# Performance work log

Hardware: AMD Instinct MI355X
Metric: run time of the kernel (lower is better)

The kernel has to match this reference:

```python
import jax, jax.numpy as jnp
import numpy as np

DIM = 1024
HEADS = 16
DIM_HEAD = 64
INNER = HEADS * DIM_HEAD
ALPHA = 128.0
SCALE = DIM_HEAD ** -0.5 / ALPHA
EPS = 1e-5
MAX_NEG = -jnp.finfo(jnp.float32).max


def layernorm(x, g):
    # torch.var(unbiased=False) layernorm with learned gain, no bias
    mean = jnp.mean(x, axis=-1, keepdims=True)
    var = jnp.mean(jnp.square(x - mean), axis=-1, keepdims=True)
    return (x - mean) * jax.lax.rsqrt(var + EPS) * g


def setup_inputs() -> dict:
    key = jax.random.key(0)
    ks = jax.random.split(key, 8)
    b, n = 8, 1024
    x = jax.random.normal(ks[0], (b, n, DIM), dtype=jnp.float32)
    mask = jax.random.bernoulli(ks[1], 0.9, (b, n))  # bool padding mask
    g_in = jnp.ones((DIM,), jnp.float32)
    Wq = jax.random.normal(ks[2], (INNER, DIM), jnp.float32) * (DIM ** -0.5)
    Wkv = jax.random.normal(ks[3], (2 * DIM_HEAD, DIM), jnp.float32) * (DIM ** -0.5)
    null_kv = jax.random.normal(ks[4], (2, DIM_HEAD), jnp.float32)
    Wo = jax.random.normal(ks[5], (DIM, INNER), jnp.float32) * (INNER ** -0.5)
    g_out = jnp.ones((DIM,), jnp.float32)
    return {"x": x, "mask": mask, "g_in": g_in, "Wq": Wq, "Wkv": Wkv,
            "null_kv": null_kv, "Wo": Wo, "g_out": g_out}


def reference(x, mask, g_in, Wq, Wkv, null_kv, Wo, g_out):
    b, n, _ = x.shape
    context = x                      # context captured BEFORE norm
    xn = layernorm(x, g_in)
    q = (xn @ Wq.T).reshape(b, n, HEADS, DIM_HEAD).transpose(0, 2, 1, 3)  # b h n d
    q = q * SCALE
    kv = context @ Wkv.T             # b n 2d (single shared KV head: MQA)
    k, v = jnp.split(kv, 2, axis=-1)
    nk = jnp.broadcast_to(null_kv[0], (b, 1, DIM_HEAD))
    nv = jnp.broadcast_to(null_kv[1], (b, 1, DIM_HEAD))
    k = jnp.concatenate([nk, k], axis=1)   # b (n+1) d
    v = jnp.concatenate([nv, v], axis=1)
    sim = jnp.einsum('bhid,bjd->bhij', q, k)  # b h n (n+1)
    # padding mask, True prepended for null token
    m = jnp.pad(mask, ((0, 0), (1, 0)), constant_values=True)
    sim = jnp.where(m[:, None, None, :], sim, MAX_NEG)
    # causal mask: triu with offset j-i+1 = 2 (null token always visible)
    i, j = n, n + 1
    causal = jnp.triu(jnp.ones((i, j), bool), j - i + 1)
    sim = jnp.where(causal, MAX_NEG, sim)
    # pb-relax: subtract detached max, rescale by alpha, softmax
    sim = sim - jax.lax.stop_gradient(jnp.max(sim, axis=-1, keepdims=True))
    attn = jax.nn.softmax(sim * ALPHA, axis=-1)
    out = jnp.einsum('bhij,bjd->bhid', attn, v)
    out = out.transpose(0, 2, 1, 3).reshape(b, n, INNER)
    out = out @ Wo.T
    return layernorm(out, g_out)
```

## Files before the change

kernel.cpp:

```cpp
#include <hip/hip_runtime.h>
#include <hip/hip_bf16.h>

#define B_     8
#define N_     1024
#define DIM_   1024
#define HEADS_ 16
#define DH_    64
#define INNER_ 1024
#define NKEY_  1025
#define NTILE_ 33
#define NW_    33
#define ROWS_  8192
#define EPS_   1e-5f
#define QK_SCALE_ 0.1803368801111f
#define TILE_ELEMS_ 4096

typedef unsigned short u16;
typedef unsigned char  u8;
typedef unsigned int   u32;
typedef __attribute__((ext_vector_type(8)))  short bf16x8;
typedef __attribute__((ext_vector_type(4)))  float f32x4;
typedef __attribute__((ext_vector_type(16))) float f32x16;

__device__ __forceinline__ float bf2f(u16 u) {
    unsigned int x = ((unsigned int)u) << 16;
    return __uint_as_float(x);
}
__device__ __forceinline__ u16 f2bf(float f) {
    unsigned int x = __float_as_uint(f);
    x += 0x7FFFu + ((x >> 16) & 1u);
    return (u16)(x >> 16);
}
__device__ __forceinline__ float max3f(float a, float b, float c) {
    return fmaxf(fmaxf(a, b), c);
}
__device__ __forceinline__ float exp2fast(float x) {
    float r;
    asm("v_exp_f32 %0, %1" : "=v"(r) : "v"(x));
    return r;
}

#define MFMA16(a, b, c) __builtin_amdgcn_mfma_f32_16x16x32_bf16((a), (b), (c), 0, 0, 0)
#define MFMA32(a, b, c) __builtin_amdgcn_mfma_f32_32x32x16_bf16((a), (b), (c), 0, 0, 0)

__device__ __forceinline__ void gload16(const void* g, void* l) {
    __builtin_amdgcn_global_load_lds(
        (const __attribute__((address_space(1))) unsigned int*)g,
        (__attribute__((address_space(3))) unsigned int*)l, 16, 0, 0);
}

__device__ __forceinline__ u32 cvtpk(float lo, float hi) {
    u32 r;
    asm("v_cvt_pk_bf16_f32 %0, %1, %2" : "=v"(r) : "v"(lo), "v"(hi));
    return r;
}
__device__ __forceinline__ void plswap(u32& a, u32& b) {
    asm volatile("v_permlane32_swap_b32 %0, %1" : "+v"(a), "+v"(b));
}

__global__ void detect_mask(const unsigned int* __restrict__ m, int* __restrict__ flag) {
    if (threadIdx.x == 0 && blockIdx.x == 0) {
        int f = 0;
        for (int i = 0; i < 64; ++i) {
            unsigned int w = m[i];
            if (w == 0x3F800000u) { f = 2; break; }
            if (w > 1u) f = 1;
        }
        *flag = f;
    }
}

__global__ void build_bits(const void* __restrict__ mraw, const int* __restrict__ flag,
                           u32* __restrict__ vbits) {
    int tid = blockIdx.x * blockDim.x + threadIdx.x;
    if (tid >= B_ * NW_) return;
    int b = tid / NW_, wq = tid - b * NW_;
    int f = *flag;
    u32 bits = 0;
    for (int i = 0; i < 32; ++i) {
        int jp = wq * 32 + i;
        bool vis;
        if (jp == 0) vis = true;
        else if (jp < NKEY_) {
            int idx = b * N_ + jp - 1;
            if (f == 0)      vis = ((const int*)mraw)[idx] != 0;
            else if (f == 1) vis = ((const u8*)mraw)[idx] != 0;
            else             vis = ((const float*)mraw)[idx] != 0.0f;
        } else vis = false;
        if (vis) bits |= (1u << i);
    }
    vbits[tid] = bits;
}

__global__ void cvt_w(const float* __restrict__ wq, const float* __restrict__ wkv,
                      const float* __restrict__ wo, u16* __restrict__ q16,
                      u16* __restrict__ kv16, u16* __restrict__ o16) {
    int i = blockIdx.x * blockDim.x + threadIdx.x;
    const int NQ = INNER_ * DIM_ / 4, NKV = 128 * DIM_ / 4, NO = DIM_ * INNER_ / 4;
    const float* src; u16* dst; int off;
    if (i < NQ)            { src = wq;  dst = q16;  off = i; }
    else if (i < NQ + NKV) { src = wkv; dst = kv16; off = i - NQ; }
    else if (i < NQ + NKV + NO) { src = wo; dst = o16; off = i - NQ - NKV; }
    else return;
    float4 v = ((const float4*)src)[off];
    ushort4 u; u.x = f2bf(v.x); u.y = f2bf(v.y); u.z = f2bf(v.z); u.w = f2bf(v.w);
    ((ushort4*)dst)[off] = u;
}

template<int MODE>
__global__ __launch_bounds__(256)
void ln_rows(const void* __restrict__ xv, const float* __restrict__ g,
             void* __restrict__ outv, u16* __restrict__ raw16) {
    int row = blockIdx.x;
    int t = threadIdx.x;
    float v0, v1, v2, v3;
    if constexpr (MODE == 0) {
        float4 v = ((const float4*)((const float*)xv + (size_t)row * DIM_))[t];
        v0 = v.x; v1 = v.y; v2 = v.z; v3 = v.w;
    } else {
        ushort4 u = ((const ushort4*)((const u16*)xv + (size_t)row * DIM_))[t];
        v0 = bf2f(u.x); v1 = bf2f(u.y); v2 = bf2f(u.z); v3 = bf2f(u.w);
    }
    float s  = v0 + v1 + v2 + v3;
    float ss = v0*v0 + v1*v1 + v2*v2 + v3*v3;
#pragma unroll
    for (int off = 32; off > 0; off >>= 1) {
        s  += __shfl_down(s,  off, 64);
        ss += __shfl_down(ss, off, 64);
    }
    __shared__ float red[10];
    int wid = t >> 6, lane = t & 63;
    if (lane == 0) { red[wid] = s; red[4 + wid] = ss; }
    __syncthreads();
    if (t == 0) {
        float S  = red[0] + red[1] + red[2] + red[3];
        float SS = red[4] + red[5] + red[6] + red[7];
        float mean = S * (1.0f / DIM_);
        float var  = SS * (1.0f / DIM_) - mean * mean;
        red[8] = mean;
        red[9] = rsqrtf(var + EPS_);
    }
    __syncthreads();
    float mean = red[8], rs = red[9];
    float4 gv = ((const float4*)g)[t];
    float o0 = (v0 - mean) * rs * gv.x;
    float o1 = (v1 - mean) * rs * gv.y;
    float o2 = (v2 - mean) * rs * gv.z;
    float o3 = (v3 - mean) * rs * gv.w;
    if constexpr (MODE == 0) {
        ushort4 u; u.x = f2bf(o0); u.y = f2bf(o1); u.z = f2bf(o2); u.w = f2bf(o3);
        ((ushort4*)((u16*)outv + (size_t)row * DIM_))[t] = u;
        ushort4 rw; rw.x = f2bf(v0); rw.y = f2bf(v1); rw.z = f2bf(v2); rw.w = f2bf(v3);
        ((ushort4*)(raw16 + (size_t)row * DIM_))[t] = rw;
    } else {
        float4 u; u.x = o0; u.y = o1; u.z = o2; u.w = o3;
        ((float4*)((float*)outv + (size_t)row * DIM_))[t] = u;
    }
}

__global__ __launch_bounds__(256)
void proj_fused(const u16* __restrict__ xn, const u16* __restrict__ xraw,
                const u16* __restrict__ wq, const u16* __restrict__ wkv,
                u16* __restrict__ qout, float* __restrict__ kvout) {
    __shared__ u16 As[128 * 32];
    __shared__ u16 Bs[128 * 32];
    const bool iskv = (blockIdx.x == 8);
    const u16* A  = iskv ? xraw : xn;
    const u16* Bt = iskv ? wkv : wq;
    const int  n0 = iskv ? 0 : blockIdx.x * 128;
    const float scale = iskv ? 1.0f : QK_SCALE_;
    const int t = threadIdx.x;
    const int w = t >> 6, l = t & 63;
    const int col = l & 15, rg = l >> 4;
    const int wm = (w >> 1) * 64, wn = (w & 1) * 64;
    const int m0 = blockIdx.y * 128;
    const int slr = l >> 2;
    const int slc = (l & 3) * 8;
    f32x4 acc[4][4];
#pragma unroll
    for (int i = 0; i < 4; ++i)
#pragma unroll
        for (int j = 0; j < 4; ++j) acc[i][j] = f32x4{0.f, 0.f, 0.f, 0.f};

    const u16* Abase = A  + (size_t)m0 * DIM_;
    const u16* Bbase = Bt + (size_t)n0 * DIM_;
    for (int k0 = 0; k0 < DIM_; k0 += 32) {
        __syncthreads();
#pragma unroll
        for (int p = 0; p < 2; ++p) {
            int rb = w * 2 + p;
            gload16(Abase + (size_t)(rb * 16 + slr) * DIM_ + k0 + slc, &As[rb * 512]);
            gload16(Bbase + (size_t)(rb * 16 + slr) * DIM_ + k0 + slc, &Bs[rb * 512]);
        }
        __syncthreads();
        bf16x8 af[4], bf4[4];
#pragma unroll
        for (int mi = 0; mi < 4; ++mi)
            af[mi] = *(const bf16x8*)&As[(wm + mi * 16 + col) * 32 + rg * 8];
#pragma unroll
        for (int ni = 0; ni < 4; ++ni)
            bf4[ni] = *(const bf16x8*)&Bs[(wn + ni * 16 + col) * 32 + rg * 8];
#pragma unroll
        for (int mi = 0; mi < 4; ++mi)
#pragma unroll
            for (int ni = 0; ni < 4; ++ni)
                acc[mi][ni] = MFMA16(af[mi], bf4[ni], acc[mi][ni]);
    }
#pragma unroll
    for (int mi = 0; mi < 4; ++mi)
#pragma unroll
        for (int ni = 0; ni < 4; ++ni)
#pragma unroll
            for (int r = 0; r < 4; ++r) {
                size_t row = (size_t)(m0 + wm + mi * 16 + rg * 4 + r);
                int c = n0 + wn + ni * 16 + col;
                float vv = acc[mi][ni][r] * scale;
                if (iskv) kvout[row * 128 + c] = vv;
                else      qout[row * INNER_ + c] = f2bf(vv);
            }
}

__global__ __launch_bounds__(256)
void gemm_o(const u16* __restrict__ A, const u16* __restrict__ Bt,
            u16* __restrict__ Cv) {
    __shared__ u16 As[128 * 32];
    __shared__ u16 Bs[128 * 32];
    const int t = threadIdx.x;
    const int w = t >> 6, l = t & 63;
    const int col = l & 15, rg = l >> 4;
    const int wm = (w >> 1) * 64, wn = (w & 1) * 64;
    const int m0 = blockIdx.y * 128, n0 = blockIdx.x * 128;
    const int slr = l >> 2;
    const int slc = (l & 3) * 8;
    f32x4 acc[4][4];
#pragma unroll
    for (int i = 0; i < 4; ++i)
#pragma unroll
        for (int j = 0; j < 4; ++j) acc[i][j] = f32x4{0.f, 0.f, 0.f, 0.f};
    const u16* Abase = A  + (size_t)m0 * INNER_;
    const u16* Bbase = Bt + (size_t)n0 * INNER_;
    for (int k0 = 0; k0 < INNER_; k0 += 32) {
        __syncthreads();
#pragma unroll
        for (int p = 0; p < 2; ++p) {
            int rb = w * 2 + p;
            gload16(Abase + (size_t)(rb * 16 + slr) * INNER_ + k0 + slc, &As[rb * 512]);
            gload16(Bbase + (size_t)(rb * 16 + slr) * INNER_ + k0 + slc, &Bs[rb * 512]);
        }
        __syncthreads();
        bf16x8 af[4], bf4[4];
#pragma unroll
        for (int mi = 0; mi < 4; ++mi)
            af[mi] = *(const bf16x8*)&As[(wm + mi * 16 + col) * 32 + rg * 8];
#pragma unroll
        for (int ni = 0; ni < 4; ++ni)
            bf4[ni] = *(const bf16x8*)&Bs[(wn + ni * 16 + col) * 32 + rg * 8];
#pragma unroll
        for (int mi = 0; mi < 4; ++mi)
#pragma unroll
            for (int ni = 0; ni < 4; ++ni)
                acc[mi][ni] = MFMA16(af[mi], bf4[ni], acc[mi][ni]);
    }
#pragma unroll
    for (int mi = 0; mi < 4; ++mi)
#pragma unroll
        for (int ni = 0; ni < 4; ++ni)
#pragma unroll
            for (int r = 0; r < 4; ++r) {
                size_t row = (size_t)(m0 + wm + mi * 16 + rg * 4 + r);
                int c = n0 + wn + ni * 16 + col;
                Cv[row * DIM_ + c] = f2bf(acc[mi][ni][r]);
            }
}

__global__ __launch_bounds__(256)
void build_kv(const float* __restrict__ kvf, const float* __restrict__ nullkv,
              u16* __restrict__ KVt) {
    const int kt = blockIdx.x, b = blockIdx.y;
    const int t = threadIdx.x;
    const int k0 = kt * 32;
    u16* base = KVt + ((size_t)b * NTILE_ + kt) * TILE_ELEMS_;
    {
        int j = t >> 3;
        int d0 = (t & 7) * 8;
        int jp = k0 + j;
        float v[8];
        if (jp == 0) {
#pragma unroll
            for (int i = 0; i < 8; ++i) v[i] = nullkv[d0 + i];
        } else if (jp <= N_) {
            const float* r = kvf + ((size_t)b * N_ + jp - 1) * 128 + d0;
            float4 a = ((const float4*)r)[0], c = ((const float4*)r)[1];
            v[0]=a.x; v[1]=a.y; v[2]=a.z; v[3]=a.w; v[4]=c.x; v[5]=c.y; v[6]=c.z; v[7]=c.w;
        } else {
#pragma unroll
            for (int i = 0; i < 8; ++i) v[i] = 0.f;
        }
        ushort4 u0, u1;
        u0.x=f2bf(v[0]); u0.y=f2bf(v[1]); u0.z=f2bf(v[2]); u0.w=f2bf(v[3]);
        u1.x=f2bf(v[4]); u1.y=f2bf(v[5]); u1.z=f2bf(v[6]); u1.w=f2bf(v[7]);
        *(ushort4*)(base + j * 64 + d0)     = u0;
        *(ushort4*)(base + j * 64 + d0 + 4) = u1;
    }
    {
        int d = t >> 2;
        int j0 = (t & 3) * 8;
        u16 o8[8];
#pragma unroll
        for (int i = 0; i < 8; ++i) {
            int jp = k0 + j0 + i;
            float val = 0.f;
            if (jp == 0) val = nullkv[64 + d];
            else if (jp <= N_) val = kvf[((size_t)b * N_ + jp - 1) * 128 + 64 + d];
            o8[i] = f2bf(val);
        }
        u16* dst = base + 2048 + d * 32 + j0;
        ushort4 u0, u1;
        u0.x=o8[0]; u0.y=o8[1]; u0.z=o8[2]; u0.w=o8[3];
        u1.x=o8[4]; u1.y=o8[5]; u1.z=o8[6]; u1.w=o8[7];
        *(ushort4*)dst = u0;
        *(ushort4*)(dst + 4) = u1;
    }
}

__device__ __forceinline__ void softmax_pv(
    f32x16& s, float& m, float& lsum, f32x16& o0, f32x16& o1,
    bool caus, int lim, const bf16x8* vf)
{
    float t0 = max3f(s[0],  s[1],  s[2]);
    float t1 = max3f(s[3],  s[4],  s[5]);
    float t2 = max3f(s[6],  s[7],  s[8]);
    float t3 = max3f(s[9],  s[10], s[11]);
    float t4 = max3f(s[12], s[13], s[14]);
    float mt = max3f(max3f(t0, t1, t2), max3f(t3, t4, s[15]), -3.0e38f);
    mt = fmaxf(mt, __shfl_xor(mt, 32, 64));
    if (!__all(mt <= m + 8.0f)) {
        float mn = fmaxf(m, mt);
        float c = exp2fast(m - mn);
        lsum *= c;
#pragma unroll
        for (int i = 0; i < 16; ++i) { o0[i] *= c; o1[i] *= c; }
        m = mn;
    }
    float p[16];
#pragma unroll
    for (int r = 0; r < 16; ++r) p[r] = exp2fast(s[r] - m);
    if (caus) {
#pragma unroll
        for (int r = 0; r < 16; ++r)
            if (((r & 3) + 8 * (r >> 2)) > lim) p[r] = 0.f;
    }
    float ls = (((p[0]+p[1])+(p[2]+p[3])) + ((p[4]+p[5])+(p[6]+p[7])))
             + (((p[8]+p[9])+(p[10]+p[11])) + ((p[12]+p[13])+(p[14]+p[15])));
    ls += __shfl_xor(ls, 32, 64);
    lsum += ls;
    u32 w0 = cvtpk(p[0],  p[1]),  w2 = cvtpk(p[4],  p[5]);  plswap(w0, w2);
    u32 w1 = cvtpk(p[2],  p[3]),  w3 = cvtpk(p[6],  p[7]);  plswap(w1, w3);
    u32 w4 = cvtpk(p[8],  p[9]),  w6 = cvtpk(p[12], p[13]); plswap(w4, w6);
    u32 w5 = cvtpk(p[10], p[11]), w7 = cvtpk(p[14], p[15]); plswap(w5, w7);
    union { u32 wd[4]; bf16x8 v; } f0, f1;
    f0.wd[0] = w0; f0.wd[1] = w1; f0.wd[2] = w2; f0.wd[3] = w3;
    f1.wd[0] = w4; f1.wd[1] = w5; f1.wd[2] = w6; f1.wd[3] = w7;
    __builtin_amdgcn_s_setprio(1);
    o0 = MFMA32(vf[0], f0.v, o0);
    o0 = MFMA32(vf[1], f1.v, o0);
    o1 = MFMA32(vf[2], f0.v, o1);
    o1 = MFMA32(vf[3], f1.v, o1);
    __builtin_amdgcn_s_setprio(0);
}

__device__ __forceinline__ void write_o(u16* __restrict__ Out, int b, int i0, int lo,
                                        int hi, int h, float lsum,
                                        const f32x16& o0, const f32x16& o1) {
    float inv = 1.0f / lsum;
    u16* ob = Out + ((size_t)(b * N_ + i0 + lo)) * INNER_ + h * DH_;
#pragma unroll
    for (int dd = 0; dd < 2; ++dd)
#pragma unroll
        for (int g = 0; g < 4; ++g) {
            int d0 = dd * 32 + 8 * g + 4 * hi;
            float e0 = (dd ? o1[4*g+0] : o0[4*g+0]) * inv;
            float e1 = (dd ? o1[4*g+1] : o0[4*g+1]) * inv;
            float e2 = (dd ? o1[4*g+2] : o0[4*g+2]) * inv;
            float e3 = (dd ? o1[4*g+3] : o0[4*g+3]) * inv;
            ushort4 u; u.x = f2bf(e0); u.y = f2bf(e1); u.z = f2bf(e2); u.w = f2bf(e3);
            *(ushort4*)(ob + d0) = u;
        }
}

__global__ __launch_bounds__(256)
void attn_un(const u16* __restrict__ Q, const u16* __restrict__ KVt,
             const u32* __restrict__ vbits, u16* __restrict__ Out) {
    const int t = threadIdx.x;
    const int w = t >> 6, l = t & 63;
    const int lo = l & 31, hi = l >> 5;
    const int fid = blockIdx.x;
    const int qt = 31 - (fid >> 5);
    const int rem = fid & 31;
    const int b = rem >> 2, hg = rem & 3;
    const int h = hg * 4 + w;
    const int i0 = qt * 32;
    const int nt = qt + 2;

    bf16x8 qf[4];
    {
        const u16* qp = Q + ((size_t)(b * N_ + i0 + lo)) * INNER_ + h * DH_ + hi * 8;
#pragma unroll
        for (int dt = 0; dt < 4; ++dt) qf[dt] = *(const bf16x8*)(qp + dt * 16);
    }
    f32x16 o0, o1;
#pragma unroll
    for (int i = 0; i < 16; ++i) { o0[i] = 0.f; o1[i] = 0.f; }
    float m = -3.0e38f, lsum = 0.f;

    const u16* tbase = KVt + (size_t)b * NTILE_ * TILE_ELEMS_;
    const u32* vbp = vbits + b * NW_;
    const int koff  = lo * 64 + hi * 8;
    const int voff0 = 2048 + lo * 32 + hi * 8;
    const int voff1 = 2048 + (lo + 32) * 32 + hi * 8;

    for (int kt = 0; kt < nt; ++kt) {
        const u16* tb = tbase + (size_t)kt * TILE_ELEMS_;
        bf16x8 kf[4], vf[4];
        kf[0] = *(const bf16x8*)(tb + koff);
        kf[1] = *(const bf16x8*)(tb + koff + 16);
        kf[2] = *(const bf16x8*)(tb + koff + 32);
        kf[3] = *(const bf16x8*)(tb + koff + 48);
        vf[0] = *(const bf16x8*)(tb + voff0);
        vf[1] = *(const bf16x8*)(tb + voff0 + 16);
        vf[2] = *(const bf16x8*)(tb + voff1);
        vf[3] = *(const bf16x8*)(tb + voff1 + 16);

        u32 vb = vbp[kt];
        union { u32 wd[4]; bf16x8 v; } bias, ones;
        bias.wd[0] = (hi == 0 && !((vb >> lo) & 1u)) ? 0xC6E0u : 0u;
        bias.wd[1] = 0; bias.wd[2] = 0; bias.wd[3] = 0;
        ones.wd[0] = (hi == 0) ? 0x3F80u : 0u;
        ones.wd[1] = 0; ones.wd[2] = 0; ones.wd[3] = 0;

        f32x16 s;
        __builtin_amdgcn_s_setprio(1);
#pragma unroll
        for (int i = 0; i < 16; ++i) s[i] = 0.f;
        s = MFMA32(kf[0], qf[0], s);
        s = MFMA32(kf[1], qf[1], s);
        s = MFMA32(kf[2], qf[2], s);
        s = MFMA32(kf[3], qf[3], s);
        s = MFMA32(bias.v, ones.v, s);
        __builtin_amdgcn_s_setprio(0);
        int lim = i0 + lo + 1 - kt * 32 - 4 * hi;
        softmax_pv(s, m, lsum, o0, o1, kt >= qt, lim, vf);
    }

    write_o(Out, b, i0, lo, hi, h, lsum, o0, o1);
}

extern "C" void kernel_launch(void* const* d_in, const int* in_sizes, int n_in,
                              void* d_out, int out_size, void* d_ws, size_t ws_size,
                              hipStream_t stream) {
    const float* x       = (const float*)d_in[0];
    const void*  maskraw = d_in[1];
    const float* g_in    = (const float*)d_in[2];
    const float* Wq      = (const float*)d_in[3];
    const float* Wkv     = (const float*)d_in[4];
    const float* nullkv  = (const float*)d_in[5];
    const float* Wo      = (const float*)d_in[6];
    const float* g_out   = (const float*)d_in[7];
    float* out = (float*)d_out;

    char* ws = (char*)d_ws;
    size_t off = 0;
    auto alloc = [&](size_t bytes) {
        void* p = ws + off;
        off += (bytes + 255) & ~(size_t)255;
        return p;
    };
    int* flag   = (int*)alloc(4);
    u32* vbits  = (u32*)alloc((size_t)B_ * NW_ * 4);
    u16* wq16   = (u16*)alloc((size_t)INNER_ * DIM_ * 2);
    u16* wkv16  = (u16*)alloc((size_t)128 * DIM_ * 2);
    u16* wo16   = (u16*)alloc((size_t)DIM_ * INNER_ * 2);
    u16* bufA   = (u16*)alloc((size_t)ROWS_ * DIM_ * 2);
    u16* xb     = (u16*)alloc((size_t)ROWS_ * DIM_ * 2);
    u16* bufC   = (u16*)alloc((size_t)ROWS_ * INNER_ * 2);
    float* kvf  = (float*)alloc((size_t)ROWS_ * 128 * 4);
    u16* KVt    = (u16*)alloc((size_t)B_ * NTILE_ * TILE_ELEMS_ * 2);

    detect_mask<<<1, 64, 0, stream>>>((const unsigned int*)maskraw, flag);
    build_bits<<<2, 256, 0, stream>>>(maskraw, flag, vbits);

    cvt_w<<<2176, 256, 0, stream>>>(Wq, Wkv, Wo, wq16, wkv16, wo16);

    ln_rows<0><<<ROWS_, 256, 0, stream>>>(x, g_in, bufA, xb);

    proj_fused<<<dim3(9, ROWS_ / 128), 256, 0, stream>>>(
        bufA, xb, wq16, wkv16, bufC, kvf);

    build_kv<<<dim3(NTILE_, B_), 256, 0, stream>>>(kvf, nullkv, KVt);

    attn_un<<<1024, 256, 0, stream>>>(bufC, KVt, vbits, bufA);

    gemm_o<<<dim3(DIM_ / 128, ROWS_ / 128), 256, 0, stream>>>(bufA, wo16, bufC);

    ln_rows<1><<<ROWS_, 256, 0, stream>>>(bufC, g_out, out, nullptr);
}
```

Baseline: 169.3 us.

## Process two KV tiles per attention iteration to interleave independent MFMA chains

The attention loop now handles two 32-key tiles per step. It interleaves two independent QK^T MFMA accumulation chains, does one shared online-softmax max/rescale for both, and issues the PV MFMAs for both tiles together. The tile count is padded to an even number (34) so the pair loop never reads out of bounds, and the softmax and output helpers are inlined. The aim is more instruction-level parallelism, fewer rescale checks and fewer loop iterations, at the cost of higher register pressure and some extra zero-padded work on the last step.

Measured after the change: 168.3 us. No clear change (-0.6%).

```diff
diff --git a/kernel.cpp b/kernel.cpp
--- a/kernel.cpp
+++ b/kernel.cpp
@@ -8,8 +8,8 @@
 #define DH_    64
 #define INNER_ 1024
 #define NKEY_  1025
-#define NTILE_ 33
-#define NW_    33
+#define NTILE_ 34
+#define NW_    34
 #define ROWS_  8192
 #define EPS_   1e-5f
 #define QK_SCALE_ 0.1803368801111f
@@ -323,71 +323,6 @@
     }
 }
 
-__device__ __forceinline__ void softmax_pv(
-    f32x16& s, float& m, float& lsum, f32x16& o0, f32x16& o1,
-    bool caus, int lim, const bf16x8* vf)
-{
-    float t0 = max3f(s[0],  s[1],  s[2]);
-    float t1 = max3f(s[3],  s[4],  s[5]);
-    float t2 = max3f(s[6],  s[7],  s[8]);
-    float t3 = max3f(s[9],  s[10], s[11]);
-    float t4 = max3f(s[12], s[13], s[14]);
-    float mt = max3f(max3f(t0, t1, t2), max3f(t3, t4, s[15]), -3.0e38f);
-    mt = fmaxf(mt, __shfl_xor(mt, 32, 64));
-    if (!__all(mt <= m + 8.0f)) {
-        float mn = fmaxf(m, mt);
-        float c = exp2fast(m - mn);
-        lsum *= c;
-#pragma unroll
-        for (int i = 0; i < 16; ++i) { o0[i] *= c; o1[i] *= c; }
-        m = mn;
-    }
-    float p[16];
-#pragma unroll
-    for (int r = 0; r < 16; ++r) p[r] = exp2fast(s[r] - m);
-    if (caus) {
-#pragma unroll
-        for (int r = 0; r < 16; ++r)
-            if (((r & 3) + 8 * (r >> 2)) > lim) p[r] = 0.f;
-    }
-    float ls = (((p[0]+p[1])+(p[2]+p[3])) + ((p[4]+p[5])+(p[6]+p[7])))
-             + (((p[8]+p[9])+(p[10]+p[11])) + ((p[12]+p[13])+(p[14]+p[15])));
-    ls += __shfl_xor(ls, 32, 64);
-    lsum += ls;
-    u32 w0 = cvtpk(p[0],  p[1]),  w2 = cvtpk(p[4],  p[5]);  plswap(w0, w2);
-    u32 w1 = cvtpk(p[2],  p[3]),  w3 = cvtpk(p[6],  p[7]);  plswap(w1, w3);
-    u32 w4 = cvtpk(p[8],  p[9]),  w6 = cvtpk(p[12], p[13]); plswap(w4, w6);
-    u32 w5 = cvtpk(p[10], p[11]), w7 = cvtpk(p[14], p[15]); plswap(w5, w7);
-    union { u32 wd[4]; bf16x8 v; } f0, f1;
-    f0.wd[0] = w0; f0.wd[1] = w1; f0.wd[2] = w2; f0.wd[3] = w3;
-    f1.wd[0] = w4; f1.wd[1] = w5; f1.wd[2] = w6; f1.wd[3] = w7;
-    __builtin_amdgcn_s_setprio(1);
-    o0 = MFMA32(vf[0], f0.v, o0);
-    o0 = MFMA32(vf[1], f1.v, o0);
-    o1 = MFMA32(vf[2], f0.v, o1);
-    o1 = MFMA32(vf[3], f1.v, o1);
-    __builtin_amdgcn_s_setprio(0);
-}
-
-__device__ __forceinline__ void write_o(u16* __restrict__ Out, int b, int i0, int lo,
-                                        int hi, int h, float lsum,
-                                        const f32x16& o0, const f32x16& o1) {
-    float inv = 1.0f / lsum;
-    u16* ob = Out + ((size_t)(b * N_ + i0 + lo)) * INNER_ + h * DH_;
-#pragma unroll
-    for (int dd = 0; dd < 2; ++dd)
-#pragma unroll
-        for (int g = 0; g < 4; ++g) {
-            int d0 = dd * 32 + 8 * g + 4 * hi;
-            float e0 = (dd ? o1[4*g+0] : o0[4*g+0]) * inv;
-            float e1 = (dd ? o1[4*g+1] : o0[4*g+1]) * inv;
-            float e2 = (dd ? o1[4*g+2] : o0[4*g+2]) * inv;
-            float e3 = (dd ? o1[4*g+3] : o0[4*g+3]) * inv;
-            ushort4 u; u.x = f2bf(e0); u.y = f2bf(e1); u.z = f2bf(e2); u.w = f2bf(e3);
-            *(ushort4*)(ob + d0) = u;
-        }
-}
-
 __global__ __launch_bounds__(256)
 void attn_un(const u16* __restrict__ Q, const u16* __restrict__ KVt,
              const u32* __restrict__ vbits, u16* __restrict__ Out) {
@@ -400,7 +335,7 @@
     const int b = rem >> 2, hg = rem & 3;
     const int h = hg * 4 + w;
     const int i0 = qt * 32;
-    const int nt = qt + 2;
+    const int nst = (qt + 3) >> 1;
 
     bf16x8 qf[4];
     {
@@ -419,40 +354,140 @@
     const int voff0 = 2048 + lo * 32 + hi * 8;
     const int voff1 = 2048 + (lo + 32) * 32 + hi * 8;
 
-    for (int kt = 0; kt < nt; ++kt) {
-        const u16* tb = tbase + (size_t)kt * TILE_ELEMS_;
-        bf16x8 kf[4], vf[4];
-        kf[0] = *(const bf16x8*)(tb + koff);
-        kf[1] = *(const bf16x8*)(tb + koff + 16);
-        kf[2] = *(const bf16x8*)(tb + koff + 32);
-        kf[3] = *(const bf16x8*)(tb + koff + 48);
-        vf[0] = *(const bf16x8*)(tb + voff0);
-        vf[1] = *(const bf16x8*)(tb + voff0 + 16);
-        vf[2] = *(const bf16x8*)(tb + voff1);
-        vf[3] = *(const bf16x8*)(tb + voff1 + 16);
-
-        u32 vb = vbp[kt];
-        union { u32 wd[4]; bf16x8 v; } bias, ones;
-        bias.wd[0] = (hi == 0 && !((vb >> lo) & 1u)) ? 0xC6E0u : 0u;
-        bias.wd[1] = 0; bias.wd[2] = 0; bias.wd[3] = 0;
+    for (int st = 0; st < nst; ++st) {
+        const int kt0 = st * 2, kt1 = st * 2 + 1;
+        const u16* tb0 = tbase + (size_t)kt0 * TILE_ELEMS_;
+        const u16* tb1 = tbase + (size_t)kt1 * TILE_ELEMS_;
+        bf16x8 kf0[4], kf1[4];
+        kf0[0] = *(const bf16x8*)(tb0 + koff);
+        kf0[1] = *(const bf16x8*)(tb0 + koff + 16);
+        kf0[2] = *(const bf16x8*)(tb0 + koff + 32);
+        kf0[3] = *(const bf16x8*)(tb0 + koff + 48);
+        kf1[0] = *(const bf16x8*)(tb1 + koff);
+        kf1[1] = *(const bf16x8*)(tb1 + koff + 16);
+        kf1[2] = *(const bf16x8*)(tb1 + koff + 32);
+        kf1[3] = *(const bf16x8*)(tb1 + koff + 48);
+
+        u32 vb0 = vbp[kt0], vb1 = vbp[kt1];
+        union { u32 wd[4]; bf16x8 v; } bias0, bias1, ones;
+        bias0.wd[0] = (hi == 0 && !((vb0 >> lo) & 1u)) ? 0xC6E0u : 0u;
+        bias0.wd[1] = 0; bias0.wd[2] = 0; bias0.wd[3] = 0;
+        bias1.wd[0] = (hi == 0 && !((vb1 >> lo) & 1u)) ? 0xC6E0u : 0u;
+        bias1.wd[1] = 0; bias1.wd[2] = 0; bias1.wd[3] = 0;
         ones.wd[0] = (hi == 0) ? 0x3F80u : 0u;
         ones.wd[1] = 0; ones.wd[2] = 0; ones.wd[3] = 0;
 
-        f32x16 s;
+        f32x16 s0, s1;
         __builtin_amdgcn_s_setprio(1);
 #pragma unroll
-        for (int i = 0; i < 16; ++i) s[i] = 0.f;
-        s = MFMA32(kf[0], qf[0], s);
-        s = MFMA32(kf[1], qf[1], s);
-        s = MFMA32(kf[2], qf[2], s);
-        s = MFMA32(kf[3], qf[3], s);
-        s = MFMA32(bias.v, ones.v, s);
+        for (int i = 0; i < 16; ++i) { s0[i] = 0.f; s1[i] = 0.f; }
+        s0 = MFMA32(kf0[0], qf[0], s0);
+        s1 = MFMA32(kf1[0], qf[0], s1);
+        s0 = MFMA32(kf0[1], qf[1], s0);
+        s1 = MFMA32(kf1[1], qf[1], s1);
+        s0 = MFMA32(kf0[2], qf[2], s0);
+        s1 = MFMA32(kf1[2], qf[2], s1);
+        s0 = MFMA32(kf0[3], qf[3], s0);
+        s1 = MFMA32(kf1[3], qf[3], s1);
+        s0 = MFMA32(bias0.v, ones.v, s0);
+        s1 = MFMA32(bias1.v, ones.v, s1);
         __builtin_amdgcn_s_setprio(0);
-        int lim = i0 + lo + 1 - kt * 32 - 4 * hi;
-        softmax_pv(s, m, lsum, o0, o1, kt >= qt, lim, vf);
-    }
-
-    write_o(Out, b, i0, lo, hi, h, lsum, o0, o1);
+
+        float t0 = max3f(s0[0],  s0[1],  s0[2]);
+        float t1 = max3f(s0[3],  s0[4],  s0[5]);
+        float t2 = max3f(s0[6],  s0[7],  s0[8]);
+        float t3 = max3f(s0[9],  s0[10], s0[11]);
+        float t4 = max3f(s0[12], s0[13], s0[14]);
+        float u0 = max3f(s1[0],  s1[1],  s1[2]);
+        float u1 = max3f(s1[3],  s1[4],  s1[5]);
+        float u2 = max3f(s1[6],  s1[7],  s1[8]);
+        float u3 = max3f(s1[9],  s1[10], s1[11]);
+        float u4 = max3f(s1[12], s1[13], s1[14]);
+        float mt = fmaxf(max3f(max3f(t0, t1, t2), max3f(t3, t4, s0[15]),
+                               max3f(u0, u1, u2)),
+                         max3f(u3, u4, s1[15]));
+        mt = fmaxf(mt, __shfl_xor(mt, 32, 64));
+        if (!__all(mt <= m + 8.0f)) {
+            float mn = fmaxf(m, mt);
+            float c = exp2fast(m - mn);
+            lsum *= c;
+#pragma unroll
+            for (int i = 0; i < 16; ++i) { o0[i] *= c; o1[i] *= c; }
+            m = mn;
+        }
+        float p0[16], p1[16];
+#pragma unroll
+        for (int r = 0; r < 16; ++r) p0[r] = exp2fast(s0[r] - m);
+#pragma unroll
+        for (int r = 0; r < 16; ++r) p1[r] = exp2fast(s1[r] - m);
+        if (kt0 >= qt) {
+            int lim0 = i0 + lo + 1 - kt0 * 32 - 4 * hi;
+#pragma unroll
+            for (int r = 0; r < 16; ++r)
+                if (((r & 3) + 8 * (r >> 2)) > lim0) p0[r] = 0.f;
+        }
+        if (kt1 >= qt) {
+            int lim1 = i0 + lo + 1 - kt1 * 32 - 4 * hi;
+#pragma unroll
+            for (int r = 0; r < 16; ++r)
+                if (((r & 3) + 8 * (r >> 2)) > lim1) p1[r] = 0.f;
+        }
+        float ls = ((((p0[0]+p0[1])+(p0[2]+p0[3])) + ((p0[4]+p0[5])+(p0[6]+p0[7])))
+                 +  (((p0[8]+p0[9])+(p0[10]+p0[11])) + ((p0[12]+p0[13])+(p0[14]+p0[15]))))
+                 + ((((p1[0]+p1[1])+(p1[2]+p1[3])) + ((p1[4]+p1[5])+(p1[6]+p1[7])))
+                 +  (((p1[8]+p1[9])+(p1[10]+p1[11])) + ((p1[12]+p1[13])+(p1[14]+p1[15]))));
+        ls += __shfl_xor(ls, 32, 64);
+        lsum += ls;
+
+        u32 a0 = cvtpk(p0[0],  p0[1]),  a2 = cvtpk(p0[4],  p0[5]);  plswap(a0, a2);
+        u32 a1 = cvtpk(p0[2],  p0[3]),  a3 = cvtpk(p0[6],  p0[7]);  plswap(a1, a3);
+        u32 a4 = cvtpk(p0[8],  p0[9]),  a6 = cvtpk(p0[12], p0[13]); plswap(a4, a6);
+        u32 a5 = cvtpk(p0[10], p0[11]), a7 = cvtpk(p0[14], p0[15]); plswap(a5, a7);
+        u32 c0 = cvtpk(p1[0],  p1[1]),  c2 = cvtpk(p1[4],  p1[5]);  plswap(c0, c2);
+        u32 c1 = cvtpk(p1[2],  p1[3]),  c3 = cvtpk(p1[6],  p1[7]);  plswap(c1, c3);
+        u32 c4 = cvtpk(p1[8],  p1[9]),  c6 = cvtpk(p1[12], p1[13]); plswap(c4, c6);
+        u32 c5 = cvtpk(p1[10], p1[11]), c7 = cvtpk(p1[14], p1[15]); plswap(c5, c7);
+        union { u32 wd[4]; bf16x8 v; } f0, f1, g0, g1;
+        f0.wd[0] = a0; f0.wd[1] = a1; f0.wd[2] = a2; f0.wd[3] = a3;
+        f1.wd[0] = a4; f1.wd[1] = a5; f1.wd[2] = a6; f1.wd[3] = a7;
+        g0.wd[0] = c0; g0.wd[1] = c1; g0.wd[2] = c2; g0.wd[3] = c3;
+        g1.wd[0] = c4; g1.wd[1] = c5; g1.wd[2] = c6; g1.wd[3] = c7;
+
+        bf16x8 vf0[4], vf1[4];
+        vf0[0] = *(const bf16x8*)(tb0 + voff0);
+        vf0[1] = *(const bf16x8*)(tb0 + voff0 + 16);
+        vf0[2] = *(const bf16x8*)(tb0 + voff1);
+        vf0[3] = *(const bf16x8*)(tb0 + voff1 + 16);
+        vf1[0] = *(const bf16x8*)(tb1 + voff0);
+        vf1[1] = *(const bf16x8*)(tb1 + voff0 + 16);
+        vf1[2] = *(const bf16x8*)(tb1 + voff1);
+        vf1[3] = *(const bf16x8*)(tb1 + voff1 + 16);
+        __builtin_amdgcn_s_setprio(1);
+        o0 = MFMA32(vf0[0], f0.v, o0);
+        o1 = MFMA32(vf0[2], f0.v, o1);
+        o0 = MFMA32(vf0[1], f1.v, o0);
+        o1 = MFMA32(vf0[3], f1.v, o1);
+        o0 = MFMA32(vf1[0], g0.v, o0);
+        o1 = MFMA32(vf1[2], g0.v, o1);
+        o0 = MFMA32(vf1[1], g1.v, o0);
+        o1 = MFMA32(vf1[3], g1.v, o1);
+        __builtin_amdgcn_s_setprio(0);
+    }
+
+    float inv = 1.0f / lsum;
+    u16* ob = Out + ((size_t)(b * N_ + i0 + lo)) * INNER_ + h * DH_;
+#pragma unroll
+    for (int dd = 0; dd < 2; ++dd)
+#pragma unroll
+        for (int g = 0; g < 4; ++g) {
+            int d0 = dd * 32 + 8 * g + 4 * hi;
+            float e0 = (dd ? o1[4*g+0] : o0[4*g+0]) * inv;
+            float e1 = (dd ? o1[4*g+1] : o0[4*g+1]) * inv;
+            float e2 = (dd ? o1[4*g+2] : o0[4*g+2]) * inv;
+            float e3 = (dd ? o1[4*g+3] : o0[4*g+3]) * inv;
+            ushort4 u; u.x = f2bf(e0); u.y = f2bf(e1); u.z = f2bf(e2); u.w = f2bf(e3);
+            *(ushort4*)(ob + d0) = u;
+        }
 }
 
 extern "C" void kernel_launch(void* const* d_in, const int* in_sizes, int n_in,
```
